# Optimization experiments

Measured on AMD Instinct MI355X. Metric: run time of the kernel, lower is better.

Reference implementation:

```python
import jax, jax.numpy as jnp
import numpy as np

jax.config.update("jax_enable_x64", True)

_FULL = 1 << 32
_MASK = _FULL - 1
_HALF = _FULL >> 1
_QUARTER = _HALF >> 1
_THREE_QUARTER = 3 * _QUARTER


def setup_inputs() -> dict:
    key = jax.random.key(0)
    num_symbols = 262144            # e.g. a 512x512 plane of {-1,+1} symbols
    num_bits = 2 * num_symbols      # compressed payload, ~2 bits/symbol budget
    payload_bits = jax.random.randint(key, (num_bits,), 0, 2, dtype=jnp.int64)
    return {
        "payload_bits": payload_bits,
        "total_freq": 4096,         # 1 << frequency_precision (12)
        "num_symbols": num_symbols,
        "context_bits": 8,
    }


def reference(payload_bits, total_freq, num_symbols, context_bits):
    bits = payload_bits.astype(jnp.int64)
    nb = bits.shape[0]
    num_states = 1 << context_bits
    smask = num_states - 1

    def read_bit(ptr):
        # _BitReader returns 0 past the end of the payload
        return jnp.where(ptr < nb, bits[jnp.clip(ptr, 0, nb - 1)], jnp.int64(0))

    # initial 32-bit code word
    idx32 = jnp.arange(32, dtype=jnp.int64)
    b32 = jnp.where(idx32 < nb, bits[jnp.clip(idx32, 0, nb - 1)], 0)
    code0 = jnp.sum(b32 << (31 - idx32))

    def renorm(carry):
        # E1/E2/E3 renormalization loop (bit-level, data dependent)
        def cond(c):
            low, high, code, ptr = c
            return (high < _HALF) | (low >= _HALF) | ((low >= _QUARTER) & (high < _THREE_QUARTER))

        def body(c):
            low, high, code, ptr = c
            sub = jnp.where(high < _HALF, jnp.int64(0),
                            jnp.where(low >= _HALF, jnp.int64(_HALF), jnp.int64(_QUARTER)))
            low = low - sub
            high = high - sub
            code = code - sub
            low = (low << 1) & _MASK
            high = ((high << 1) & _MASK) | 1
            code = ((code << 1) & _MASK) | read_bit(ptr)
            return (low, high, code, ptr + 1)

        return jax.lax.while_loop(cond, body, carry)

    def step(carry, _):
        low, high, code, ptr, state, count0, count1 = carry
        n0 = count0[state]
        n1 = count1[state]
        total = n0 + n1
        p0 = n0.astype(jnp.float64) / total.astype(jnp.float64)
        p0_freq = jnp.clip(jnp.rint(p0 * (total_freq - 2)) + 1.0, 1.0, float(total_freq - 1)).astype(jnp.int64)
        rng = high - low + 1                      # fits int64 (<= 2^32)
        scaled = ((code - low + 1) * total_freq - 1) // rng
        split = low + rng * p0_freq // total_freq
        bit = (scaled >= p0_freq).astype(jnp.int64)
        low2 = jnp.where(bit == 0, low, split)
        high2 = jnp.where(bit == 0, split - 1, high)
        low3, high3, code3, ptr3 = renorm((low2, high2, code, ptr))
        count0 = count0.at[state].add(1 - bit)
        count1 = count1.at[state].add(bit)
        state2 = ((state << 1) | bit) & smask
        return (low3, high3, code3, ptr3, state2, count0, count1), bit

    init = (
        jnp.int64(0),               # low
        jnp.int64(_MASK),           # high = 2^32 - 1
        code0.astype(jnp.int64),    # code
        jnp.int64(32),              # bit pointer (32 bits consumed)
        jnp.int64(0),               # context state
        jnp.ones(num_states, dtype=jnp.int64),  # count0 (Laplace init)
        jnp.ones(num_states, dtype=jnp.int64),  # count1
    )
    _, out_bits = jax.lax.scan(step, init, None, length=num_symbols)
    # map {0,1} -> {-1,+1} float32 symbols (reshape to bitstream.shape is metadata-only)
    return out_bits.astype(jnp.float32) * 2.0 - 1.0
```

## Files before the change

kernel.cpp:

```cpp
#include <hip/hip_runtime.h>


#define WORDS_LDS 16400
#define MAX_STATES 1024

__device__ __forceinline__ long long ddiv_floor(long long n, long long d) {
    double qd = (double)n / (double)d;
    long long q = (long long)qd;
    long long r = n - q * d;
    q -= (r < 0);
    q += (r >= d);
    return q;
}

template<bool POW2>
__device__ __forceinline__ void decode_serial(
    const unsigned* __restrict__ words, unsigned* tab,
    const int* __restrict__ bits, int nb, int nwords,
    unsigned total_freq, int tf_shift, int num_symbols, int smask,
    unsigned pf0, float* __restrict__ out)
{
    const unsigned H = 0x80000000u;
    unsigned low = 0u, high = 0xFFFFFFFFu;
    unsigned code = words[0];
    unsigned long long bitbuf = (((unsigned long long)words[1]) << 32) | (unsigned long long)words[2];
    int navail = 64;
    unsigned pre = words[3];
    int widx = 4;

    const double tfm2d = (double)(total_freq - 2u);
    const int tfm1 = (int)(total_freq - 1u);

    int state = 0;
    unsigned n0 = 1u, n1 = 1u, pf = pf0;

    int wIdx = 0;
    unsigned wN0 = 1u, wN1 = 1u, wPf = pf0;

    float* op = out;

    for (int s = 0; s < num_symbols; ++s) {
        const int c0 = (state << 1) & smask;
        uint4 q = *reinterpret_cast<const uint4*>(tab + 2 * c0);

        if (navail <= 32) {
            bitbuf |= ((unsigned long long)pre) << (32 - navail);
            navail += 32;
            unsigned nxt = 0u;
            if (widx < WORDS_LDS) {
                nxt = words[widx];
            } else if (widx < nwords) {
                unsigned g = 0u;
                long long base = ((long long)widx) << 5;
                for (int j = 0; j < 32; ++j) {
                    long long idx = base + j;
                    int b = (idx < (long long)nb) ? (bits[idx] & 1) : 0;
                    g |= ((unsigned)b) << (31 - j);
                }
                nxt = g;
            }
            pre = nxt;
            ++widx;
        }

        const unsigned rngm1 = high - low;
        const unsigned long long P = (unsigned long long)pf * rngm1 + pf;
        const unsigned dlt = code - low;
        const unsigned long long N = POW2
            ? ((((unsigned long long)dlt) << tf_shift) + (unsigned long long)tfm1)
            : ((unsigned long long)dlt * total_freq + (unsigned long long)(total_freq - 1u));
        const int bit = (N >= P) ? 1 : 0;
        const unsigned soff = POW2 ? (unsigned)(P >> tf_shift)
                                   : (unsigned)ddiv_floor((long long)P, (long long)total_freq);
        const unsigned split = low + soff;
        low  = bit ? split : low;
        high = bit ? high : (split - 1u);
        *op++ = bit ? 1.0f : -1.0f;

        const unsigned nn0 = n0 + (unsigned)(1 - bit);
        const unsigned nn1 = n1 + (unsigned)bit;
        double p0d = (double)(int)nn0 / (double)(int)(nn0 + nn1);
        double pfd = rint(p0d * tfm2d) + 1.0;
        int pfi = (int)pfd;
        pfi = pfi < 1 ? 1 : (pfi > tfm1 ? tfm1 : pfi);
        const unsigned pfn = (unsigned)pfi;

        const unsigned x = low ^ high;
        const int k = __builtin_clz(x);
        const unsigned aa = ~(low << (k + 1));
        const unsigned bb = (high << (k + 1)) | ((2u << k) - 1u);
        const int ca = __builtin_clz(aa);
        const int cb = __builtin_clz(bb);
        const int m = ca < cb ? ca : cb;
        const int K = k + m;
        const unsigned sub = (m != 0) ? H : 0u;
        const unsigned ones = (1u << K) - 1u;
        const unsigned t13 = (unsigned)(bitbuf >> 51);
        const unsigned tK = t13 >> (13 - K);
        low  = (low << K) - sub;
        high = (high << K) + ones - sub;
        code = ((code << K) | tK) - sub;
        bitbuf <<= K;
        navail -= K;

        const int nidx = c0 | bit;
        const unsigned sw0 = bit ? q.z : q.x;
        const unsigned sw1 = bit ? q.w : q.y;
        const bool f2 = (nidx == wIdx);
        unsigned xn0 = f2 ? wN0 : sw0;
        unsigned xn1 = f2 ? wN1 : (sw1 & 0xFFFFFu);
        unsigned xpf = f2 ? wPf : (sw1 >> 20);

        *reinterpret_cast<uint2*>(tab + 2 * wIdx) = make_uint2(wN0, wN1 | (wPf << 20));

        wIdx = state; wN0 = nn0; wN1 = nn1; wPf = pfn;

        if (__builtin_expect(nidx == state, 0)) {
            asm volatile("");
            xn0 = nn0; xn1 = nn1; xpf = pfn;
        }
        state = nidx;
        n0 = xn0; n1 = xn1; pf = xpf;
    }
}

__global__ __launch_bounds__(256)
void EntropyDecoder_84928683311460_kernel(
    const int* __restrict__ bits,
    const int* __restrict__ tf_p,
    const int* __restrict__ ns_p,
    const int* __restrict__ cb_p,
    float* __restrict__ out,
    int nb)
{
    __shared__ unsigned words[WORDS_LDS];
    __shared__ __align__(16) unsigned tab[MAX_STATES * 2];

    const int tid = threadIdx.x;
    const unsigned total_freq = (unsigned)(*tf_p);
    const int num_symbols = *ns_p;
    const int context_bits = *cb_p;
    const int num_states = 1 << context_bits;
    const int smask = num_states - 1;
    const int nwords = (nb + 31) >> 5;

    for (int w = tid; w < WORDS_LDS; w += blockDim.x) {
        unsigned v = 0;
        int base = w << 5;
        if (base + 32 <= nb) {
            #pragma unroll
            for (int j = 0; j < 32; j += 4) {
                int4 b4 = *reinterpret_cast<const int4*>(bits + base + j);
                v |= ((unsigned)(b4.x & 1) << (31 - j))
                   | ((unsigned)(b4.y & 1) << (30 - j))
                   | ((unsigned)(b4.z & 1) << (29 - j))
                   | ((unsigned)(b4.w & 1) << (28 - j));
            }
        } else if (base < nb) {
            for (int j = 0; j < 32; ++j) {
                int idx = base + j;
                int b = (idx < nb) ? (bits[idx] & 1) : 0;
                v |= ((unsigned)b) << (31 - j);
            }
        }
        words[w] = v;
    }
    unsigned pf0;
    {
        double pfd = rint(0.5 * (double)(total_freq - 2u)) + 1.0;
        int t = (int)pfd;
        int tfm1 = (int)(total_freq - 1u);
        t = t < 1 ? 1 : (t > tfm1 ? tfm1 : t);
        pf0 = (unsigned)t;
    }
    for (int st = tid; st < num_states; st += blockDim.x) {
        tab[2 * st]     = 1u;
        tab[2 * st + 1] = 1u | (pf0 << 20);
    }
    __syncthreads();
    if (tid != 0) return;

    const int tf_shift = 31 - __builtin_clz(total_freq);
    if ((total_freq & (total_freq - 1u)) == 0u)
        decode_serial<true >(words, tab, bits, nb, nwords, total_freq, tf_shift,
                             num_symbols, smask, pf0, out);
    else
        decode_serial<false>(words, tab, bits, nb, nwords, total_freq, tf_shift,
                             num_symbols, smask, pf0, out);
}

extern "C" void kernel_launch(void* const* d_in, const int* in_sizes, int n_in,
                              void* d_out, int out_size, void* d_ws, size_t ws_size,
                              hipStream_t stream) {
    const int* bits = (const int*)d_in[0];
    const int* tf   = (const int*)d_in[1];
    const int* ns   = (const int*)d_in[2];
    const int* cb   = (const int*)d_in[3];
    float* out = (float*)d_out;
    int nb = in_sizes[0];

    hipLaunchKernelGGL(EntropyDecoder_84928683311460_kernel,
                       dim3(1), dim3(256), 0, stream,
                       bits, tf, ns, cb, out, nb);
}
```

Before: 81.13 ms.

## Replace f64 probability update with float-reciprocal integer path and buffer output bits in LDS

Within the serial decode loop, the per-symbol f64 divide and rint are replaced by an integer rounding computed with a float reciprocal plus a correction step. The exact f64 path is kept as a fallback for exact ties. The bit decision now compares the offset directly against the split offset, and the renormalization clz min is merged into a single clz. Decoded bits are packed into 32-bit words in shared memory, and all threads expand them to floats after the loop, which takes per-symbol global stores off the single-thread critical path. The fast path only runs under bounds chosen so the integer arithmetic cannot overflow.

```diff
diff --git a/kernel.cpp b/kernel.cpp
--- a/kernel.cpp
+++ b/kernel.cpp
@@ -3,6 +3,7 @@
 
 #define WORDS_LDS 16400
 #define MAX_STATES 1024
+#define OBITS_WORDS 8192
 
 __device__ __forceinline__ long long ddiv_floor(long long n, long long d) {
     double qd = (double)n / (double)d;
@@ -13,9 +14,9 @@
     return q;
 }
 
-template<bool POW2>
+template<bool FAST>
 __device__ __forceinline__ void decode_serial(
-    const unsigned* __restrict__ words, unsigned* tab,
+    const unsigned* __restrict__ words, unsigned* tab, unsigned* obits,
     const int* __restrict__ bits, int nb, int nwords,
     unsigned total_freq, int tf_shift, int num_symbols, int smask,
     unsigned pf0, float* __restrict__ out)
@@ -30,6 +31,8 @@
 
     const double tfm2d = (double)(total_freq - 2u);
     const int tfm1 = (int)(total_freq - 1u);
+    const unsigned tfm2_2 = (total_freq - 2u) << 1;
+    constexpr int EXT = FAST ? 14 : 30;
 
     int state = 0;
     unsigned n0 = 1u, n1 = 1u, pf = pf0;
@@ -37,7 +40,7 @@
     int wIdx = 0;
     unsigned wN0 = 1u, wN1 = 1u, wPf = pf0;
 
-    float* op = out;
+    unsigned obuf = 0u;
 
     for (int s = 0; s < num_symbols; ++s) {
         const int c0 = (state << 1) & smask;
@@ -65,38 +68,54 @@
 
         const unsigned rngm1 = high - low;
         const unsigned long long P = (unsigned long long)pf * rngm1 + pf;
+        const unsigned soff = FAST ? (unsigned)(P >> tf_shift)
+                                   : (unsigned)ddiv_floor((long long)P, (long long)total_freq);
         const unsigned dlt = code - low;
-        const unsigned long long N = POW2
-            ? ((((unsigned long long)dlt) << tf_shift) + (unsigned long long)tfm1)
-            : ((unsigned long long)dlt * total_freq + (unsigned long long)(total_freq - 1u));
-        const int bit = (N >= P) ? 1 : 0;
-        const unsigned soff = POW2 ? (unsigned)(P >> tf_shift)
-                                   : (unsigned)ddiv_floor((long long)P, (long long)total_freq);
+        const int bit = (dlt >= soff) ? 1 : 0;
         const unsigned split = low + soff;
         low  = bit ? split : low;
         high = bit ? high : (split - 1u);
-        *op++ = bit ? 1.0f : -1.0f;
+        obuf = (obuf << 1) | (unsigned)bit;
 
         const unsigned nn0 = n0 + (unsigned)(1 - bit);
         const unsigned nn1 = n1 + (unsigned)bit;
-        double p0d = (double)(int)nn0 / (double)(int)(nn0 + nn1);
-        double pfd = rint(p0d * tfm2d) + 1.0;
-        int pfi = (int)pfd;
-        pfi = pfi < 1 ? 1 : (pfi > tfm1 ? tfm1 : pfi);
-        const unsigned pfn = (unsigned)pfi;
+        unsigned pfn;
+        if (FAST) {
+            const unsigned t  = nn0 + nn1;
+            const unsigned d2 = t << 1;
+            const unsigned num2 = __umul24(tfm2_2, nn0) + t;
+            const float qf = (float)num2 * __builtin_amdgcn_rcpf((float)d2);
+            unsigned qi = (unsigned)qf;
+            int r = (int)(num2 - __umul24(qi, d2));
+            if (r < 0)          { qi -= 1u; r += (int)d2; }
+            if (r >= (int)d2)   { qi += 1u; r -= (int)d2; }
+            pfn = qi + 1u;
+            if (__builtin_expect(r == 0, 0)) {
+                asm volatile("");
+                double p0d = (double)(int)nn0 / (double)(int)t;
+                double pfd = rint(p0d * tfm2d) + 1.0;
+                int pfi = (int)pfd;
+                pfi = pfi < 1 ? 1 : (pfi > tfm1 ? tfm1 : pfi);
+                pfn = (unsigned)pfi;
+            }
+        } else {
+            double p0d = (double)(int)nn0 / (double)(int)(nn0 + nn1);
+            double pfd = rint(p0d * tfm2d) + 1.0;
+            int pfi = (int)pfd;
+            pfi = pfi < 1 ? 1 : (pfi > tfm1 ? tfm1 : pfi);
+            pfn = (unsigned)pfi;
+        }
 
         const unsigned x = low ^ high;
         const int k = __builtin_clz(x);
         const unsigned aa = ~(low << (k + 1));
         const unsigned bb = (high << (k + 1)) | ((2u << k) - 1u);
-        const int ca = __builtin_clz(aa);
-        const int cb = __builtin_clz(bb);
-        const int m = ca < cb ? ca : cb;
+        const int m = __builtin_clz(aa | bb);
         const int K = k + m;
         const unsigned sub = (m != 0) ? H : 0u;
         const unsigned ones = (1u << K) - 1u;
-        const unsigned t13 = (unsigned)(bitbuf >> 51);
-        const unsigned tK = t13 >> (13 - K);
+        const unsigned tE = (unsigned)(bitbuf >> (64 - EXT));
+        const unsigned tK = tE >> (EXT - K);
         low  = (low << K) - sub;
         high = (high << K) + ones - sub;
         code = ((code << K) | tK) - sub;
@@ -112,7 +131,6 @@
         unsigned xpf = f2 ? wPf : (sw1 >> 20);
 
         *reinterpret_cast<uint2*>(tab + 2 * wIdx) = make_uint2(wN0, wN1 | (wPf << 20));
-
         wIdx = state; wN0 = nn0; wN1 = nn1; wPf = pfn;
 
         if (__builtin_expect(nidx == state, 0)) {
@@ -121,6 +139,29 @@
         }
         state = nidx;
         n0 = xn0; n1 = xn1; pf = xpf;
+
+        if ((s & 31) == 31) {
+            int wo = s >> 5;
+            if (wo < OBITS_WORDS) {
+                obits[wo] = obuf;
+            } else {
+                int base = s & ~31;
+                for (int j = 0; j < 32; ++j)
+                    out[base + j] = ((obuf >> (31 - j)) & 1u) ? 1.0f : -1.0f;
+            }
+        }
+    }
+    if (num_symbols & 31) {
+        int rem = num_symbols & 31;
+        unsigned v = obuf << (32 - rem);
+        int wo = num_symbols >> 5;
+        if (wo < OBITS_WORDS) {
+            obits[wo] = v;
+        } else {
+            int base = num_symbols & ~31;
+            for (int j = 0; j < rem; ++j)
+                out[base + j] = ((v >> (31 - j)) & 1u) ? 1.0f : -1.0f;
+        }
     }
 }
 
@@ -135,6 +176,7 @@
 {
     __shared__ unsigned words[WORDS_LDS];
     __shared__ __align__(16) unsigned tab[MAX_STATES * 2];
+    __shared__ unsigned obits[OBITS_WORDS];
 
     const int tid = threadIdx.x;
     const unsigned total_freq = (unsigned)(*tf_p);
@@ -178,15 +220,44 @@
         tab[2 * st + 1] = 1u | (pf0 << 20);
     }
     __syncthreads();
-    if (tid != 0) return;
-
-    const int tf_shift = 31 - __builtin_clz(total_freq);
-    if ((total_freq & (total_freq - 1u)) == 0u)
-        decode_serial<true >(words, tab, bits, nb, nwords, total_freq, tf_shift,
-                             num_symbols, smask, pf0, out);
-    else
-        decode_serial<false>(words, tab, bits, nb, nwords, total_freq, tf_shift,
-                             num_symbols, smask, pf0, out);
+
+    if (tid == 0) {
+        const int tf_shift = 31 - __builtin_clz(total_freq);
+        const bool pow2 = (total_freq & (total_freq - 1u)) == 0u;
+        const unsigned long long bound =
+            2ull * (unsigned long long)(total_freq - 2u) * (unsigned long long)(num_symbols + 1)
+            + (unsigned long long)(num_symbols + 2);
+        const bool fast = pow2 && total_freq >= 8u && total_freq <= 4096u
+                          && bound < (1ull << 31);
+        if (fast)
+            decode_serial<true >(words, tab, obits, bits, nb, nwords, total_freq,
+                                 tf_shift, num_symbols, smask, pf0, out);
+        else
+            decode_serial<false>(words, tab, obits, bits, nb, nwords, total_freq,
+                                 tf_shift, num_symbols, smask, pf0, out);
+    }
+    __syncthreads();
+
+    const int nwout = (num_symbols + 31) >> 5;
+    const int npk = nwout < OBITS_WORDS ? nwout : OBITS_WORDS;
+    for (int w = tid; w < npk; w += blockDim.x) {
+        unsigned v = obits[w];
+        int base = w << 5;
+        if (base + 32 <= num_symbols) {
+            #pragma unroll
+            for (int j = 0; j < 32; j += 4) {
+                float4 o;
+                o.x = ((v >> (31 - j)) & 1u) ? 1.0f : -1.0f;
+                o.y = ((v >> (30 - j)) & 1u) ? 1.0f : -1.0f;
+                o.z = ((v >> (29 - j)) & 1u) ? 1.0f : -1.0f;
+                o.w = ((v >> (28 - j)) & 1u) ? 1.0f : -1.0f;
+                *reinterpret_cast<float4*>(out + base + j) = o;
+            }
+        } else {
+            for (int j = 0; j < 32 && base + j < num_symbols; ++j)
+                out[base + j] = ((v >> (31 - j)) & 1u) ? 1.0f : -1.0f;
+        }
+    }
 }
 
 extern "C" void kernel_launch(void* const* d_in, const int* in_sizes, int n_in,
```

New measurement: 79.84 ms. No clear change (-1.6%).
